# Kernel tuning notes

Measured on AMD Instinct MI355X. Metric: run time of the kernel, lower is better.

The kernel has to match this reference:

```python
import jax, jax.numpy as jnp
import numpy as np

WINDOW = 25  # causal sliding-window size for trend extraction


def setup_inputs() -> dict:
    key = jax.random.key(0)
    kx, kw1, kb1, kw2, kb2 = jax.random.split(key, 5)
    T = 720
    bound = 1.0 / np.sqrt(T)
    x = jax.random.normal(kx, (32, 512, T), dtype=jnp.float32)
    trend_w = jax.random.uniform(kw1, (T, T), jnp.float32, -bound, bound)
    trend_b = jax.random.uniform(kb1, (T,), jnp.float32, -bound, bound)
    seasonal_w = jax.random.uniform(kw2, (T, T), jnp.float32, -bound, bound)
    seasonal_b = jax.random.uniform(kb2, (T,), jnp.float32, -bound, bound)
    return {"x": x, "trend_w": trend_w, "trend_b": trend_b,
            "seasonal_w": seasonal_w, "seasonal_b": seasonal_b}


def _causal_window_mean(x, window):
    # x: [B, N, T]; trend[..., j] = mean(x[..., max(0, j-window+1):j+1])
    T = x.shape[-1]
    cs = jnp.cumsum(x, axis=-1)
    cs_shift = jnp.concatenate(
        [jnp.zeros(x.shape[:-1] + (window,), x.dtype), cs[..., :T - window]], axis=-1)
    counts = jnp.minimum(jnp.arange(T) + 1, window).astype(x.dtype)
    return (cs - cs_shift) / counts


def reference(x, trend_w, trend_b, seasonal_w, seasonal_b):
    trend = _causal_window_mean(x, WINDOW)
    seasonal = x - trend
    trend_out = jnp.einsum('bnt,ut->bnu', trend, trend_w) + trend_b
    seasonal_out = jnp.einsum('bnt,ut->bnu', seasonal, seasonal_w) + seasonal_b
    return trend_out + seasonal_out
```

## Files before the change

### kernel.cpp

```cpp
#include <hip/hip_runtime.h>
#include <hip/hip_bf16.h>


#define Tdim  720
#define KP    736
#define WROWS 768
#define NK    23
#define BM    64
#define APAD  744

using bf16x8 = __attribute__((ext_vector_type(8))) __bf16;
using f32x4  = __attribute__((ext_vector_type(4))) float;

__global__ void fold_w_kernel(const float* __restrict__ tw,
                              const float* __restrict__ tb,
                              const float* __restrict__ sw,
                              const float* __restrict__ sb,
                              __bf16* __restrict__ Wb,
                              float* __restrict__ beff) {
  int idx = blockIdx.x * 256 + threadIdx.x;
  if (idx >= WROWS * KP) return;
  int u = idx / KP;
  int i = idx - u * KP;
  float w = 0.0f;
  if (u < Tdim && i < Tdim) {
    const float* twr = tw + (size_t)u * Tdim;
    const float* swr = sw + (size_t)u * Tdim;
    int tend = (i + 25 < Tdim) ? (i + 25) : Tdim;
    float acc = 0.0f;
    if (i >= 24) {
      #pragma unroll 5
      for (int t = i; t < tend; ++t) acc += twr[t] - swr[t];
      acc *= 0.04f;
    } else {
      for (int t = i; t < tend; ++t) {
        float c = (t >= 24) ? 0.04f : 1.0f / (float)(t + 1);
        acc += (twr[t] - swr[t]) * c;
      }
    }
    w = swr[i] + acc;
  }
  Wb[idx] = (__bf16)w;
  if (i == 0 && u < Tdim) beff[u] = tb[u] + sb[u];
}

__global__ __launch_bounds__(1024, 1)
void dlinear_gemm(const float* __restrict__ x,
                  const __bf16* __restrict__ Wb,
                  const float* __restrict__ beff,
                  float* __restrict__ out) {
  __shared__ __bf16 As[BM * APAD];

  const int tid  = threadIdx.x;
  const int lane = tid & 63;
  const int wid  = tid >> 6;
  const int lg = lane >> 4, lr = lane & 15;

  const int m0 = blockIdx.x * BM;
  const int u0 = wid * 48;

  #pragma unroll
  for (int c = 0; c < 6; ++c) {
    int idx = tid + 1024 * c;
    if (idx < BM * 90) {
      int row  = idx / 90;
      int col8 = idx - row * 90;
      const float* p = x + (size_t)(m0 + row) * Tdim + col8 * 8;
      f32x4 a0 = ((const f32x4*)p)[0];
      f32x4 a1 = ((const f32x4*)p)[1];
      bf16x8 v;
      #pragma unroll
      for (int j = 0; j < 4; ++j) { v[j] = (__bf16)a0[j]; v[j + 4] = (__bf16)a1[j]; }
      *(bf16x8*)(&As[row * APAD + col8 * 8]) = v;
    }
  }
  {
    int r = tid >> 4;
    int c = 720 + (tid & 15);
    As[r * APAD + c] = (__bf16)0.0f;
  }
  __syncthreads();

  const __bf16* wp[3];
  #pragma unroll
  for (int ni = 0; ni < 3; ++ni)
    wp[ni] = Wb + (size_t)(u0 + ni * 16 + lr) * KP + lg * 8;

  int arofs[4];
  #pragma unroll
  for (int mi = 0; mi < 4; ++mi) arofs[mi] = (mi * 16 + lr) * APAD + lg * 8;

  f32x4 acc[4][3];
  #pragma unroll
  for (int mi = 0; mi < 4; ++mi)
    #pragma unroll
    for (int ni = 0; ni < 3; ++ni) {
      f32x4 z; z[0] = 0.f; z[1] = 0.f; z[2] = 0.f; z[3] = 0.f;
      acc[mi][ni] = z;
    }

  bf16x8 s0[3], s1[3], s2[3];
  #pragma unroll
  for (int ni = 0; ni < 3; ++ni) s0[ni] = *(const bf16x8*)(wp[ni]);
  #pragma unroll
  for (int ni = 0; ni < 3; ++ni) s1[ni] = *(const bf16x8*)(wp[ni] + 32);

#define GEMM_STEP(T, SLOT, ISSUE_SLOT, DO_ISSUE)                               \
  {                                                                            \
    if (DO_ISSUE) {                                                            \
      _Pragma("unroll")                                                        \
      for (int ni = 0; ni < 3; ++ni)                                           \
        ISSUE_SLOT[ni] = *(const bf16x8*)(wp[ni] + ((T) + 2) * 32);            \
    }                                                                          \
    bf16x8 av[4];                                                              \
    _Pragma("unroll")                                                          \
    for (int mi = 0; mi < 4; ++mi)                                             \
      av[mi] = *(const bf16x8*)(&As[arofs[mi] + (T) * 32]);                    \
    _Pragma("unroll")                                                          \
    for (int mi = 0; mi < 4; ++mi)                                             \
      _Pragma("unroll")                                                        \
      for (int ni = 0; ni < 3; ++ni)                                           \
        acc[mi][ni] = __builtin_amdgcn_mfma_f32_16x16x32_bf16(av[mi],          \
                        SLOT[ni], acc[mi][ni], 0, 0, 0);                       \
  }

  for (int t = 0; t < 21; t += 3) {
    GEMM_STEP(t,     s0, s2, true)
    GEMM_STEP(t + 1, s1, s0, true)
    GEMM_STEP(t + 2, s2, s1, true)
  }
  GEMM_STEP(21, s0, s2, false)
  GEMM_STEP(22, s1, s2, false)
#undef GEMM_STEP

  #pragma unroll
  for (int ni = 0; ni < 3; ++ni) {
    const int u = u0 + ni * 16 + lr;
    if (u >= Tdim) continue;
    const float bias = beff[u];
    #pragma unroll
    for (int mi = 0; mi < 4; ++mi) {
      const int mb = m0 + mi * 16 + lg * 4;
      #pragma unroll
      for (int j = 0; j < 4; ++j)
        out[(size_t)(mb + j) * Tdim + u] = acc[mi][ni][j] + bias;
    }
  }
}

extern "C" void kernel_launch(void* const* d_in, const int* in_sizes, int n_in,
                              void* d_out, int out_size, void* d_ws, size_t ws_size,
                              hipStream_t stream) {
  const float* x  = (const float*)d_in[0];
  const float* tw = (const float*)d_in[1];
  const float* tb = (const float*)d_in[2];
  const float* sw = (const float*)d_in[3];
  const float* sb = (const float*)d_in[4];
  float* out = (float*)d_out;

  __bf16* Wb  = (__bf16*)d_ws;
  float* beff = (float*)((char*)d_ws + (size_t)WROWS * KP * sizeof(__bf16));

  const int fold_total = WROWS * KP;
  fold_w_kernel<<<dim3((fold_total + 255) / 256), dim3(256), 0, stream>>>(
      tw, tb, sw, sb, Wb, beff);

  const int M = in_sizes[0] / Tdim;
  dim3 grid(M / BM);
  dlinear_gemm<<<grid, dim3(1024), 0, stream>>>(x, Wb, beff, out);
}
```

Baseline: 46.75 us.

## Split GEMM blocks across N halves and K halves for higher occupancy

Each block now covers half of the output columns with 512 threads instead of all 768 columns with 1024 threads, so the grid doubles. The A tile is staged in shared memory in two K-halves of 384, which cuts LDS per block so up to four blocks can share a CU. W prefetch depth drops from two steps to one. The cost is that each x tile is read and converted twice (once per column half), plus extra barriers between the K-halves.

```diff
diff --git a/kernel.cpp b/kernel.cpp
--- a/kernel.cpp
+++ b/kernel.cpp
@@ -5,9 +5,9 @@
 #define Tdim  720
 #define KP    736
 #define WROWS 768
-#define NK    23
 #define BM    64
-#define APAD  744
+#define KH    384
+#define KHPAD 396
 
 using bf16x8 = __attribute__((ext_vector_type(8))) __bf16;
 using f32x4  = __attribute__((ext_vector_type(4))) float;
@@ -44,42 +44,48 @@
   if (i == 0 && u < Tdim) beff[u] = tb[u] + sb[u];
 }
 
-__global__ __launch_bounds__(1024, 1)
+__global__ __launch_bounds__(512, 4)
 void dlinear_gemm(const float* __restrict__ x,
                   const __bf16* __restrict__ Wb,
                   const float* __restrict__ beff,
                   float* __restrict__ out) {
-  __shared__ __bf16 As[BM * APAD];
+  __shared__ __bf16 As[BM * KHPAD];
 
   const int tid  = threadIdx.x;
   const int lane = tid & 63;
   const int wid  = tid >> 6;
   const int lg = lane >> 4, lr = lane & 15;
 
-  const int m0 = blockIdx.x * BM;
-  const int u0 = wid * 48;
-
-  #pragma unroll
-  for (int c = 0; c < 6; ++c) {
-    int idx = tid + 1024 * c;
-    if (idx < BM * 90) {
-      int row  = idx / 90;
-      int col8 = idx - row * 90;
-      const float* p = x + (size_t)(m0 + row) * Tdim + col8 * 8;
-      f32x4 a0 = ((const f32x4*)p)[0];
-      f32x4 a1 = ((const f32x4*)p)[1];
-      bf16x8 v;
-      #pragma unroll
-      for (int j = 0; j < 4; ++j) { v[j] = (__bf16)a0[j]; v[j + 4] = (__bf16)a1[j]; }
-      *(bf16x8*)(&As[row * APAD + col8 * 8]) = v;
-    }
-  }
-  {
-    int r = tid >> 4;
-    int c = 720 + (tid & 15);
-    As[r * APAD + c] = (__bf16)0.0f;
-  }
-  __syncthreads();
+  const int mblk  = blockIdx.x >> 1;
+  const int nhalf = blockIdx.x & 1;
+  const int m0 = mblk * BM;
+  const int u0 = nhalf * 384 + wid * 48;
+
+#define STAGE_HALF(H)                                                          \
+  {                                                                            \
+    _Pragma("unroll")                                                          \
+    for (int c = 0; c < 6; ++c) {                                              \
+      int idx  = tid + 512 * c;                                                \
+      int row  = idx / 48;                                                     \
+      int col8 = idx - row * 48;                                               \
+      if ((H) == 0 || col8 < 42) {                                             \
+        const float* p = x + (size_t)(m0 + row) * Tdim + (H) * KH + col8 * 8;  \
+        f32x4 a0 = ((const f32x4*)p)[0];                                       \
+        f32x4 a1 = ((const f32x4*)p)[1];                                       \
+        bf16x8 v;                                                              \
+        _Pragma("unroll")                                                      \
+        for (int j = 0; j < 4; ++j) {                                          \
+          v[j] = (__bf16)a0[j]; v[j + 4] = (__bf16)a1[j];                      \
+        }                                                                      \
+        *(bf16x8*)(&As[row * KHPAD + col8 * 8]) = v;                           \
+      } else if (col8 < 44) {                                                  \
+        bf16x8 v;                                                              \
+        _Pragma("unroll")                                                      \
+        for (int j = 0; j < 8; ++j) v[j] = (__bf16)0.0f;                       \
+        *(bf16x8*)(&As[row * KHPAD + col8 * 8]) = v;                           \
+      }                                                                        \
+    }                                                                          \
+  }
 
   const __bf16* wp[3];
   #pragma unroll
@@ -88,7 +94,7 @@
 
   int arofs[4];
   #pragma unroll
-  for (int mi = 0; mi < 4; ++mi) arofs[mi] = (mi * 16 + lr) * APAD + lg * 8;
+  for (int mi = 0; mi < 4; ++mi) arofs[mi] = (mi * 16 + lr) * KHPAD + lg * 8;
 
   f32x4 acc[4][3];
   #pragma unroll
@@ -99,18 +105,14 @@
       acc[mi][ni] = z;
     }
 
-  bf16x8 s0[3], s1[3], s2[3];
-  #pragma unroll
-  for (int ni = 0; ni < 3; ++ni) s0[ni] = *(const bf16x8*)(wp[ni]);
-  #pragma unroll
-  for (int ni = 0; ni < 3; ++ni) s1[ni] = *(const bf16x8*)(wp[ni] + 32);
-
-#define GEMM_STEP(T, SLOT, ISSUE_SLOT, DO_ISSUE)                               \
+  bf16x8 sA[3], sB[3];
+
+#define KSTEP(T, CUR, NXT, DO_LOAD, HOFF)                                      \
   {                                                                            \
-    if (DO_ISSUE) {                                                            \
+    if (DO_LOAD) {                                                             \
       _Pragma("unroll")                                                        \
       for (int ni = 0; ni < 3; ++ni)                                           \
-        ISSUE_SLOT[ni] = *(const bf16x8*)(wp[ni] + ((T) + 2) * 32);            \
+        NXT[ni] = *(const bf16x8*)(wp[ni] + (HOFF) + ((T) + 1) * 32);          \
     }                                                                          \
     bf16x8 av[4];                                                              \
     _Pragma("unroll")                                                          \
@@ -121,17 +123,44 @@
       _Pragma("unroll")                                                        \
       for (int ni = 0; ni < 3; ++ni)                                           \
         acc[mi][ni] = __builtin_amdgcn_mfma_f32_16x16x32_bf16(av[mi],          \
-                        SLOT[ni], acc[mi][ni], 0, 0, 0);                       \
-  }
-
-  for (int t = 0; t < 21; t += 3) {
-    GEMM_STEP(t,     s0, s2, true)
-    GEMM_STEP(t + 1, s1, s0, true)
-    GEMM_STEP(t + 2, s2, s1, true)
-  }
-  GEMM_STEP(21, s0, s2, false)
-  GEMM_STEP(22, s1, s2, false)
-#undef GEMM_STEP
+                        CUR[ni], acc[mi][ni], 0, 0, 0);                        \
+  }
+
+  STAGE_HALF(0)
+  __syncthreads();
+  #pragma unroll
+  for (int ni = 0; ni < 3; ++ni) sA[ni] = *(const bf16x8*)(wp[ni]);
+  KSTEP(0,  sA, sB, true,  0)
+  KSTEP(1,  sB, sA, true,  0)
+  KSTEP(2,  sA, sB, true,  0)
+  KSTEP(3,  sB, sA, true,  0)
+  KSTEP(4,  sA, sB, true,  0)
+  KSTEP(5,  sB, sA, true,  0)
+  KSTEP(6,  sA, sB, true,  0)
+  KSTEP(7,  sB, sA, true,  0)
+  KSTEP(8,  sA, sB, true,  0)
+  KSTEP(9,  sB, sA, true,  0)
+  KSTEP(10, sA, sB, true,  0)
+  KSTEP(11, sB, sA, false, 0)
+  __syncthreads();
+
+  STAGE_HALF(1)
+  __syncthreads();
+  #pragma unroll
+  for (int ni = 0; ni < 3; ++ni) sA[ni] = *(const bf16x8*)(wp[ni] + KH);
+  KSTEP(0,  sA, sB, true,  KH)
+  KSTEP(1,  sB, sA, true,  KH)
+  KSTEP(2,  sA, sB, true,  KH)
+  KSTEP(3,  sB, sA, true,  KH)
+  KSTEP(4,  sA, sB, true,  KH)
+  KSTEP(5,  sB, sA, true,  KH)
+  KSTEP(6,  sA, sB, true,  KH)
+  KSTEP(7,  sB, sA, true,  KH)
+  KSTEP(8,  sA, sB, true,  KH)
+  KSTEP(9,  sB, sA, true,  KH)
+  KSTEP(10, sA, sB, false, KH)
+#undef KSTEP
+#undef STAGE_HALF
 
   #pragma unroll
   for (int ni = 0; ni < 3; ++ni) {
@@ -166,6 +195,6 @@
       tw, tb, sw, sb, Wb, beff);
 
   const int M = in_sizes[0] / Tdim;
-  dim3 grid(M / BM);
-  dlinear_gemm<<<grid, dim3(1024), 0, stream>>>(x, Wb, beff, out);
+  dim3 grid((M / BM) * 2);
+  dlinear_gemm<<<grid, dim3(512), 0, stream>>>(x, Wb, beff, out);
 }
```

Result: slower. 51.30 us (+9.7%).
